# Optimization experiments

Measured on AMD Instinct MI355X. Metric: run time of the kernel, lower is better.

Reference implementation:

```python
import jax, jax.numpy as jnp
import numpy as np

N = 50000   # nodes of the target node type
E = 800000  # edges per incoming edge type (avg degree 16)
D = 128     # in == hidden == out channels (required by the module's pooling layer)


def sage_mean(x, edge_index, Wl, bl, Wr):
    """PyG SAGEConv with mean aggregation: lin_l(mean_j x_j) + lin_r(x_i).
    Note: per the original code, sources are gathered from the TARGET node
    feature table (x_input = x_dict[tgt_node_type])."""
    src, tgt = edge_index[0], edge_index[1]
    msg = x[src]                                                   # [E, D] gather
    agg = jax.ops.segment_sum(msg, tgt, num_segments=x.shape[0])   # [N, D] scatter-add
    cnt = jax.ops.segment_sum(jnp.ones((edge_index.shape[1],), x.dtype), tgt,
                              num_segments=x.shape[0])             # [N] degree
    agg = agg / jnp.maximum(cnt, 1.0)[:, None]                     # mean; 0 for isolated nodes
    return agg @ Wl + bl + x @ Wr                                  # [N, D]


def setup_inputs() -> dict:
    key = jax.random.key(0)
    ks = jax.random.split(key, 6)
    s = 1.0 / np.sqrt(D)
    x = jax.random.normal(ks[0], (N, D), jnp.float32)
    edge_index_a = jax.random.randint(ks[1], (2, E), 0, N)
    edge_index_b = jax.random.randint(ks[2], (2, E), 0, N)
    Wl = jax.random.normal(ks[3], (D, D), jnp.float32) * s
    Wr = jax.random.normal(ks[4], (D, D), jnp.float32) * s
    bl = jnp.zeros((D,), jnp.float32)
    Wp = jax.random.normal(ks[5], (D, D), jnp.float32) * s
    bp = jnp.zeros((D,), jnp.float32)
    return {"x": x, "Wl": Wl, "bl": bl, "Wr": Wr, "Wp": Wp, "bp": bp,
            "edge_index_a": edge_index_a, "edge_index_b": edge_index_b}


def reference(x, Wl, bl, Wr, Wp, bp, edge_index_a, edge_index_b):
    # One SAGEConv encoder + pooling Linear shared across incoming edge types,
    # softmax per edge type, then mean over edge types (torch.stack(...).mean(0)).
    outs = []
    for ei in (edge_index_a, edge_index_b):
        h = sage_mean(x, ei, Wl, bl, Wr)            # [N, D]
        outs.append(jax.nn.softmax(h @ Wp + bp, axis=-1))
    return (outs[0] + outs[1]) * 0.5                # [N, D]
```

## Files before the change

kernel.cpp:

```cpp
#include <hip/hip_runtime.h>
#include <math.h>

constexpr int D    = 128;
constexpr int BT   = 128;
constexpr int TILE = 4096;

using bf16x8 = __attribute__((ext_vector_type(8))) short;
using f32x4  = __attribute__((ext_vector_type(4))) float;
#define MFMA16 __builtin_amdgcn_mfma_f32_16x16x32_bf16

__device__ __forceinline__ unsigned short f2bf(float f) {
    unsigned u = __builtin_bit_cast(unsigned, f);
    u = (u + 0x7FFF + ((u >> 16) & 1)) >> 16;
    return (unsigned short)u;
}

__global__ __launch_bounds__(256)
void prep_kernel(const float* __restrict__ x, unsigned short* __restrict__ x_bfs,
                 const int* __restrict__ ea, int Ea,
                 const int* __restrict__ eb, int Eb,
                 unsigned int* __restrict__ ent_a, int* __restrict__ cnt_a,
                 unsigned int* __restrict__ ent_b, int* __restrict__ cnt_b,
                 const float* __restrict__ Wl, const float* __restrict__ Wr,
                 const float* __restrict__ Wp,
                 unsigned short* __restrict__ WlB, unsigned short* __restrict__ WrB,
                 unsigned short* __restrict__ WpB,
                 int N, int NBKT, int CAP, int GA, int GB, int GCONV)
{
    __shared__ int hist[512];
    __shared__ int base[512];

    const int bid = blockIdx.x;
    const int t   = threadIdx.x;

    if (bid < GA + GB) {
        const int type = (bid >= GA);
        const int* e   = type ? eb : ea;
        const int  E   = type ? Eb : Ea;
        unsigned int* ent = type ? ent_b : ent_a;
        int* cnt          = type ? cnt_b : cnt_a;
        const int i0 = (bid - type * GA) * TILE;

        for (int h = t; h < NBKT; h += 256) hist[h] = 0;
        __syncthreads();

        int tgts[16];
        #pragma unroll
        for (int j = 0; j < 16; ++j) {
            int i = i0 + j * 256 + t;
            tgts[j] = (i < E) ? e[(size_t)E + i] : -1;
            if (tgts[j] >= 0) atomicAdd(&hist[tgts[j] >> 7], 1);
        }
        __syncthreads();

        for (int h = t; h < NBKT; h += 256) {
            base[h] = (hist[h] > 0) ? atomicAdd(&cnt[h], hist[h]) : 0;
            hist[h] = 0;
        }
        __syncthreads();

        #pragma unroll
        for (int j = 0; j < 16; ++j) {
            int i = i0 + j * 256 + t;
            if (tgts[j] >= 0) {
                int b   = tgts[j] >> 7;
                int pos = base[b] + atomicAdd(&hist[b], 1);
                if (pos < CAP)
                    ent[(size_t)b * CAP + pos] = ((unsigned)e[i] << 7) | (tgts[j] & 127);
            }
        }
    } else if (bid < GA + GB + GCONV) {
        const int total4 = N * 32;
        for (int i = (bid - GA - GB) * 256 + t; i < total4; i += GCONV * 256) {
            int n  = i >> 5;
            int j4 = i & 31;
            float4 v = reinterpret_cast<const float4*>(x)[i];
            ushort4 o;
            o.x = f2bf(v.x); o.y = f2bf(v.y); o.z = f2bf(v.z); o.w = f2bf(v.w);
            int s = j4 >> 3, c = (j4 & 7) * 4;
            *reinterpret_cast<ushort4*>(x_bfs + ((size_t)s * N + n) * 32 + c) = o;
        }
    } else {
        int gw = ((bid - GA - GB - GCONV) * 256 + t) >> 6;
        int l  = t & 63;
        const float* W = (gw < 32) ? Wl : (gw < 64) ? Wr : Wp;
        unsigned short* O = (gw < 32) ? WlB : (gw < 64) ? WrB : WpB;
        int ktnt = gw & 31, kt = ktnt >> 3, nt = ktnt & 7;
        bf16x8 v;
        #pragma unroll
        for (int j = 0; j < 8; ++j)
            v[j] = (short)f2bf(W[(size_t)(kt * 32 + (l >> 4) * 8 + j) * D + nt * 16 + (l & 15)]);
        *reinterpret_cast<bf16x8*>(O + ((size_t)ktnt * 64 + l) * 8) = v;
    }
}

__global__ __launch_bounds__(512)
void sort_kernel(const unsigned int* __restrict__ ent_a, const int* __restrict__ cnt_a,
                 const unsigned int* __restrict__ ent_b, const int* __restrict__ cnt_b,
                 unsigned short* __restrict__ srcl_g, int* __restrict__ off_g,
                 int NBKT, int CAP)
{
    extern __shared__ __align__(16) char smem_raw[];
    int* tmp  = (int*)smem_raw;
    int* off  = tmp + CAP;
    int* cur  = off + BT + 1;
    int* wtot = cur + BT;
    unsigned short* srcl = (unsigned short*)(wtot + 2);

    const int bid  = blockIdx.x;
    const int type = (bid >= NBKT);
    const int k    = bid - type * NBKT;
    const unsigned int* ent = type ? ent_b : ent_a;
    const int cnt = min((type ? cnt_b : cnt_a)[k], CAP);

    const int t = threadIdx.x, l = t & 63, w = t >> 6;

    if (t < BT) off[t] = 0;
    __syncthreads();

    for (int i = t; i < cnt; i += 512) {
        unsigned e = ent[(size_t)k * CAP + i];
        tmp[i] = (int)e;
        atomicAdd(&off[e & (BT - 1)], 1);
    }
    __syncthreads();

    int v = 0, s = 0;
    if (t < BT) {
        v = off[t]; s = v;
        #pragma unroll
        for (int o = 1; o < 64; o <<= 1) {
            int u = __shfl_up(s, o, 64);
            if (l >= o) s += u;
        }
        if (l == 63) wtot[w] = s;
    }
    __syncthreads();
    if (t < BT) {
        int ex = ((w == 1) ? wtot[0] : 0) + s - v;
        off[t] = ex; cur[t] = ex;
    }
    if (t == 0) off[BT] = wtot[0] + wtot[1];
    __syncthreads();

    for (int i = t; i < cnt; i += 512) {
        unsigned e = (unsigned)tmp[i];
        int pos = atomicAdd(&cur[e & (BT - 1)], 1);
        srcl[pos] = (unsigned short)(e >> 7);
    }
    __syncthreads();

    for (int i = t; i < cnt; i += 512)
        srcl_g[(size_t)bid * CAP + i] = srcl[i];
    if (t <= BT)
        off_g[(size_t)bid * (BT + 1) + t] = off[t];
}

__global__ __launch_bounds__(256)
void gather_kernel(const unsigned short* __restrict__ x_bfs,
                   const unsigned short* __restrict__ srcl_g,
                   const int* __restrict__ off_g,
                   unsigned short* __restrict__ mean_a_s,
                   unsigned short* __restrict__ mean_b_s,
                   int N, int NBKT, int CAP)
{
    extern __shared__ __align__(16) char smem_raw[];
    int* off = (int*)smem_raw;
    unsigned short* srcl = (unsigned short*)(off + BT + 1);

    const int bid   = blockIdx.x;
    const int slice = bid & 3;
    const int tb    = bid >> 2;
    const int type  = (tb >= NBKT);
    const int k     = tb - type * NBKT;

    const int t = threadIdx.x, l = t & 63, w = t >> 6;
    const int q = l >> 4, c = l & 15;

    const int cnt = off_g[(size_t)tb * (BT + 1) + BT];
    for (int i = t; i <= BT; i += 256)
        off[i] = off_g[(size_t)tb * (BT + 1) + i];
    for (int i = t; i < cnt; i += 256)
        srcl[i] = srcl_g[(size_t)tb * CAP + i];
    __syncthreads();

    const unsigned short* xs = x_bfs + (size_t)slice * N * 32;
    unsigned short* mean = (type ? mean_b_s : mean_a_s) + (size_t)slice * N * 32;

    for (int tt = w; tt < BT; tt += 4) {
        const int n = k * BT + tt;
        if (n >= N) break;
        const int o0 = off[tt], o1 = off[tt + 1];
        float ax = 0.f, ay = 0.f;

        int j = o0 + q;
        for (; j + 4 < o1; j += 8) {
            int s0 = srcl[j], s1 = srcl[j + 4];
            unsigned v0 = *(const unsigned*)(xs + (size_t)s0 * 32 + c * 2);
            unsigned v1 = *(const unsigned*)(xs + (size_t)s1 * 32 + c * 2);
            ax += __builtin_bit_cast(float, v0 << 16)
                + __builtin_bit_cast(float, v1 << 16);
            ay += __builtin_bit_cast(float, v0 & 0xffff0000u)
                + __builtin_bit_cast(float, v1 & 0xffff0000u);
        }
        if (j < o1) {
            int s0 = srcl[j];
            unsigned v0 = *(const unsigned*)(xs + (size_t)s0 * 32 + c * 2);
            ax += __builtin_bit_cast(float, v0 << 16);
            ay += __builtin_bit_cast(float, v0 & 0xffff0000u);
        }

        ax += __shfl_xor(ax, 16, 64); ax += __shfl_xor(ax, 32, 64);
        ay += __shfl_xor(ay, 16, 64); ay += __shfl_xor(ay, 32, 64);

        float r = 1.0f / fmaxf((float)(o1 - o0), 1.0f);
        if (q == 0) {
            unsigned o = ((unsigned)f2bf(ay * r) << 16) | f2bf(ax * r);
            *(unsigned*)(mean + (size_t)n * 32 + c * 2) = o;
        }
    }
}

__global__ __launch_bounds__(256)
void gemm_kernel(const unsigned short* __restrict__ mean_a_s,
                 const unsigned short* __restrict__ mean_b_s,
                 const unsigned short* __restrict__ x_bfs,
                 const unsigned short* __restrict__ WlB,
                 const unsigned short* __restrict__ WrB,
                 const unsigned short* __restrict__ WpB,
                 const float* __restrict__ bl, const float* __restrict__ bp,
                 float* __restrict__ out, int N)
{
    __shared__ unsigned short hA[64 * D];
    __shared__ unsigned short hB[64 * D];

    const int t = threadIdx.x, w = t >> 6, l = t & 63;
    const int q = l & 15;
    const int kg = l >> 4;
    const int node0 = blockIdx.x * 64 + w * 16;
    const int arow = min(node0 + q, N - 1);

    bf16x8 fa[4], fb[4], fx[4];
    #pragma unroll
    for (int kt = 0; kt < 4; ++kt) {
        size_t o = ((size_t)kt * N + arow) * 32 + kg * 8;
        fa[kt] = *reinterpret_cast<const bf16x8*>(mean_a_s + o);
        fb[kt] = *reinterpret_cast<const bf16x8*>(mean_b_s + o);
        fx[kt] = *reinterpret_cast<const bf16x8*>(x_bfs + o);
    }

    #pragma unroll
    for (int nt = 0; nt < 8; ++nt) {
        f32x4 ca = {0.f, 0.f, 0.f, 0.f};
        f32x4 cb = {0.f, 0.f, 0.f, 0.f};
        #pragma unroll
        for (int kt = 0; kt < 4; ++kt) {
            const size_t fo = ((size_t)(kt * 8 + nt) * 64 + l) * 8;
            bf16x8 wl = *reinterpret_cast<const bf16x8*>(WlB + fo);
            bf16x8 wr = *reinterpret_cast<const bf16x8*>(WrB + fo);
            ca = MFMA16(fa[kt], wl, ca, 0, 0, 0);
            ca = MFMA16(fx[kt], wr, ca, 0, 0, 0);
            cb = MFMA16(fb[kt], wl, cb, 0, 0, 0);
            cb = MFMA16(fx[kt], wr, cb, 0, 0, 0);
        }
        float blv = bl[nt * 16 + q];
        #pragma unroll
        for (int r = 0; r < 4; ++r) {
            int lrow = w * 16 + kg * 4 + r;
            int byte = lrow * 256 + (nt * 16 + q) * 2;
            byte ^= ((lrow & 7) << 4);
            *reinterpret_cast<unsigned short*>(reinterpret_cast<char*>(hA) + byte) = f2bf(ca[r] + blv);
            *reinterpret_cast<unsigned short*>(reinterpret_cast<char*>(hB) + byte) = f2bf(cb[r] + blv);
        }
    }
    __syncthreads();

    bf16x8 ga[4], gb[4];
    #pragma unroll
    for (int kt = 0; kt < 4; ++kt) {
        int lrow = w * 16 + q;
        int byte = lrow * 256 + kt * 64 + kg * 16;
        byte ^= ((lrow & 7) << 4);
        ga[kt] = *reinterpret_cast<bf16x8*>(reinterpret_cast<char*>(hA) + byte);
        gb[kt] = *reinterpret_cast<bf16x8*>(reinterpret_cast<char*>(hB) + byte);
    }

    f32x4 la[8], lb[8];
    #pragma unroll
    for (int nt = 0; nt < 8; ++nt) {
        la[nt] = f32x4{0.f, 0.f, 0.f, 0.f};
        lb[nt] = f32x4{0.f, 0.f, 0.f, 0.f};
        #pragma unroll
        for (int kt = 0; kt < 4; ++kt) {
            const size_t fo = ((size_t)(kt * 8 + nt) * 64 + l) * 8;
            bf16x8 wp = *reinterpret_cast<const bf16x8*>(WpB + fo);
            la[nt] = MFMA16(ga[kt], wp, la[nt], 0, 0, 0);
            lb[nt] = MFMA16(gb[kt], wp, lb[nt], 0, 0, 0);
        }
        float bpv = bp[nt * 16 + q];
        #pragma unroll
        for (int r = 0; r < 4; ++r) { la[nt][r] += bpv; lb[nt][r] += bpv; }
    }

    #pragma unroll
    for (int r = 0; r < 4; ++r) {
        float ma = -INFINITY, mb = -INFINITY;
        #pragma unroll
        for (int nt = 0; nt < 8; ++nt) {
            ma = fmaxf(ma, la[nt][r]);
            mb = fmaxf(mb, lb[nt][r]);
        }
        #pragma unroll
        for (int o = 1; o < 16; o <<= 1) {
            ma = fmaxf(ma, __shfl_xor(ma, o, 64));
            mb = fmaxf(mb, __shfl_xor(mb, o, 64));
        }
        float ea[8], eb[8], sa = 0.f, sb = 0.f;
        #pragma unroll
        for (int nt = 0; nt < 8; ++nt) {
            ea[nt] = __expf(la[nt][r] - ma); sa += ea[nt];
            eb[nt] = __expf(lb[nt][r] - mb); sb += eb[nt];
        }
        #pragma unroll
        for (int o = 1; o < 16; o <<= 1) {
            sa += __shfl_xor(sa, o, 64);
            sb += __shfl_xor(sb, o, 64);
        }
        float ra = 0.5f / sa, rb = 0.5f / sb;
        int grow = node0 + kg * 4 + r;
        if (grow < N) {
            float* o = out + (size_t)grow * D + q;
            #pragma unroll
            for (int nt = 0; nt < 8; ++nt)
                o[nt * 16] = ea[nt] * ra + eb[nt] * rb;
        }
    }
}

extern "C" void kernel_launch(void* const* d_in, const int* in_sizes, int n_in,
                              void* d_out, int out_size, void* d_ws, size_t ws_size,
                              hipStream_t stream)
{
    const float* x  = (const float*)d_in[0];
    const float* Wl = (const float*)d_in[1];
    const float* bl = (const float*)d_in[2];
    const float* Wr = (const float*)d_in[3];
    const float* Wp = (const float*)d_in[4];
    const float* bp = (const float*)d_in[5];
    const int*   ea = (const int*)d_in[6];
    const int*   eb = (const int*)d_in[7];

    const int N  = in_sizes[0] / D;
    const int Ea = in_sizes[6] / 2;
    const int Eb = in_sizes[7] / 2;

    const int NBKT = (N + BT - 1) / BT;
    const int Emax = Ea > Eb ? Ea : Eb;
    int CAP = (int)(((long long)Emax * BT / N) * 5 / 4 + 128);
    CAP = (CAP + 7) & ~7;

    unsigned int* ent_a = (unsigned int*)d_ws;
    unsigned int* ent_b = ent_a + (size_t)NBKT * CAP;
    int* cnt_a = (int*)(ent_b + (size_t)NBKT * CAP);
    int* cnt_b = cnt_a + NBKT;
    int* off_g = cnt_b + NBKT;
    uintptr_t p = (uintptr_t)(off_g + (size_t)2 * NBKT * (BT + 1));
    p = (p + 15) & ~(uintptr_t)15;
    unsigned short* srcl_g  = (unsigned short*)p;
    unsigned short* x_bfs   = srcl_g + (size_t)2 * NBKT * CAP;
    unsigned short* mean_a_s = x_bfs + (size_t)N * D;
    unsigned short* mean_b_s = mean_a_s + (size_t)N * D;
    unsigned short* WlB     = mean_b_s + (size_t)N * D;
    unsigned short* WrB     = WlB + D * D;
    unsigned short* WpB     = WrB + D * D;

    hipMemsetAsync(cnt_a, 0, sizeof(int) * 2 * (size_t)NBKT, stream);

    const int GA = (Ea + TILE - 1) / TILE;
    const int GB = (Eb + TILE - 1) / TILE;
    const int GCONV = 512;
    prep_kernel<<<GA + GB + GCONV + 24, 256, 0, stream>>>(
        x, x_bfs, ea, Ea, eb, Eb, ent_a, cnt_a, ent_b, cnt_b,
        Wl, Wr, Wp, WlB, WrB, WpB, N, NBKT, CAP, GA, GB, GCONV);

    const int smem_sort = CAP * 6 + (BT + 1 + BT + 2) * 4 + 16;
    sort_kernel<<<2 * NBKT, 512, smem_sort, stream>>>(
        ent_a, cnt_a, ent_b, cnt_b, srcl_g, off_g, NBKT, CAP);

    const int smem_gather = (BT + 1) * 4 + CAP * 2 + 16;
    gather_kernel<<<8 * NBKT, 256, smem_gather, stream>>>(
        x_bfs, srcl_g, off_g, mean_a_s, mean_b_s, N, NBKT, CAP);

    gemm_kernel<<<(N + 63) / 64, 256, 0, stream>>>(
        mean_a_s, mean_b_s, x_bfs, WlB, WrB, WpB, bl, bp, (float*)d_out, N);
}
```

Before: 150.7 us.

## Fold Wp into SAGE weights and aggregate projected features instead of raw x

Precomputes Wl·Wp and Wr·Wp (plus folded bias) in a small kernel, so each node's features are projected once by a dense GEMM before aggregation. Because mean aggregation is linear, the gather now averages projected rows, and a light epilogue only adds the root term and applies the softmax. The large second GEMM stage and the per-type duplicated GEMMs are removed. It adds an extra kernel launch and intermediate bf16 buffers, and the gather is restructured so each wave handles four nodes in lockstep up to the maximum degree. Rounding the fused weights and projected features to bf16 may change numerics slightly.

Measured after the change: 176.2 us. +16.9%, slower.

```diff
diff --git a/kernel.cpp b/kernel.cpp
--- a/kernel.cpp
+++ b/kernel.cpp
@@ -16,15 +16,65 @@
 }
 
 __global__ __launch_bounds__(256)
-void prep_kernel(const float* __restrict__ x, unsigned short* __restrict__ x_bfs,
+void wprod_kernel(const float* __restrict__ Wl, const float* __restrict__ Wr,
+                  const float* __restrict__ Wp,
+                  const float* __restrict__ bl, const float* __restrict__ bp,
+                  unsigned short* __restrict__ WlpB, unsigned short* __restrict__ WrpB,
+                  float* __restrict__ cvec)
+{
+    __shared__ float wm[128 * 128];
+    __shared__ float wp[128 * 128];
+
+    const float* Wm = blockIdx.x ? Wr : Wl;
+    unsigned short* OB = blockIdx.x ? WrpB : WlpB;
+    const int t = threadIdx.x;
+
+    for (int i = t; i < 4096; i += 256) {
+        reinterpret_cast<float4*>(wm)[i] = reinterpret_cast<const float4*>(Wm)[i];
+        reinterpret_cast<float4*>(wp)[i] = reinterpret_cast<const float4*>(Wp)[i];
+    }
+    __syncthreads();
+
+    const int w = t >> 6, l = t & 63;
+    const int r0 = w * 32 + (l >> 4) * 8;
+    const int c0 = l & 15;
+
+    float acc[8][8];
+    #pragma unroll
+    for (int j = 0; j < 8; ++j)
+        #pragma unroll
+        for (int nt = 0; nt < 8; ++nt) acc[j][nt] = 0.f;
+
+    for (int k = 0; k < 128; ++k) {
+        float wpv[8];
+        #pragma unroll
+        for (int nt = 0; nt < 8; ++nt) wpv[nt] = wp[k * 128 + nt * 16 + c0];
+        #pragma unroll
+        for (int j = 0; j < 8; ++j) {
+            float wmv = wm[(r0 + j) * 128 + k];
+            #pragma unroll
+            for (int nt = 0; nt < 8; ++nt) acc[j][nt] += wmv * wpv[nt];
+        }
+    }
+    #pragma unroll
+    for (int nt = 0; nt < 8; ++nt)
+        #pragma unroll
+        for (int j = 0; j < 8; ++j)
+            OB[((size_t)(w * 8 + nt) * 64 + l) * 8 + j] = f2bf(acc[j][nt]);
+
+    if (blockIdx.x == 0 && t < 128) {
+        float s = bp[t];
+        for (int k = 0; k < 128; ++k) s += bl[k] * wp[k * 128 + t];
+        cvec[t] = s;
+    }
+}
+
+__global__ __launch_bounds__(256)
+void prep_kernel(const float* __restrict__ x, unsigned short* __restrict__ x_bf,
                  const int* __restrict__ ea, int Ea,
                  const int* __restrict__ eb, int Eb,
                  unsigned int* __restrict__ ent_a, int* __restrict__ cnt_a,
                  unsigned int* __restrict__ ent_b, int* __restrict__ cnt_b,
-                 const float* __restrict__ Wl, const float* __restrict__ Wr,
-                 const float* __restrict__ Wp,
-                 unsigned short* __restrict__ WlB, unsigned short* __restrict__ WrB,
-                 unsigned short* __restrict__ WpB,
                  int N, int NBKT, int CAP, int GA, int GB, int GCONV)
 {
     __shared__ int hist[512];
@@ -69,28 +119,14 @@
                     ent[(size_t)b * CAP + pos] = ((unsigned)e[i] << 7) | (tgts[j] & 127);
             }
         }
-    } else if (bid < GA + GB + GCONV) {
+    } else {
         const int total4 = N * 32;
         for (int i = (bid - GA - GB) * 256 + t; i < total4; i += GCONV * 256) {
-            int n  = i >> 5;
-            int j4 = i & 31;
             float4 v = reinterpret_cast<const float4*>(x)[i];
             ushort4 o;
             o.x = f2bf(v.x); o.y = f2bf(v.y); o.z = f2bf(v.z); o.w = f2bf(v.w);
-            int s = j4 >> 3, c = (j4 & 7) * 4;
-            *reinterpret_cast<ushort4*>(x_bfs + ((size_t)s * N + n) * 32 + c) = o;
-        }
-    } else {
-        int gw = ((bid - GA - GB - GCONV) * 256 + t) >> 6;
-        int l  = t & 63;
-        const float* W = (gw < 32) ? Wl : (gw < 64) ? Wr : Wp;
-        unsigned short* O = (gw < 32) ? WlB : (gw < 64) ? WrB : WpB;
-        int ktnt = gw & 31, kt = ktnt >> 3, nt = ktnt & 7;
-        bf16x8 v;
-        #pragma unroll
-        for (int j = 0; j < 8; ++j)
-            v[j] = (short)f2bf(W[(size_t)(kt * 32 + (l >> 4) * 8 + j) * D + nt * 16 + (l & 15)]);
-        *reinterpret_cast<bf16x8*>(O + ((size_t)ktnt * 64 + l) * 8) = v;
+            reinterpret_cast<ushort4*>(x_bf)[i] = o;
+        }
     }
 }
 
@@ -157,11 +193,55 @@
 }
 
 __global__ __launch_bounds__(256)
-void gather_kernel(const unsigned short* __restrict__ x_bfs,
+void gemmz_kernel(const unsigned short* __restrict__ x_bf,
+                  const unsigned short* __restrict__ WlpB,
+                  const unsigned short* __restrict__ WrpB,
+                  const float* __restrict__ cvec,
+                  unsigned short* __restrict__ zl, unsigned short* __restrict__ zr,
+                  int N)
+{
+    const int t = threadIdx.x, w = t >> 6, l = t & 63;
+    const int q = l & 15, kg = l >> 4;
+    const int node0 = blockIdx.x * 64 + w * 16;
+    const int arow = min(node0 + q, N - 1);
+
+    bf16x8 fx[4];
+    #pragma unroll
+    for (int kt = 0; kt < 4; ++kt)
+        fx[kt] = *reinterpret_cast<const bf16x8*>(x_bf + (size_t)arow * D + kt * 32 + kg * 8);
+
+    #pragma unroll
+    for (int nt = 0; nt < 8; ++nt) {
+        f32x4 cl = {0.f, 0.f, 0.f, 0.f};
+        f32x4 cr = {0.f, 0.f, 0.f, 0.f};
+        #pragma unroll
+        for (int kt = 0; kt < 4; ++kt) {
+            const size_t fo = ((size_t)(kt * 8 + nt) * 64 + l) * 8;
+            bf16x8 wl = *reinterpret_cast<const bf16x8*>(WlpB + fo);
+            bf16x8 wr = *reinterpret_cast<const bf16x8*>(WrpB + fo);
+            cl = MFMA16(fx[kt], wl, cl, 0, 0, 0);
+            cr = MFMA16(fx[kt], wr, cr, 0, 0, 0);
+        }
+        float cv = cvec[nt * 16 + q];
+        const int sidx = nt >> 1;
+        const int cin  = (nt & 1) * 16 + q;
+        #pragma unroll
+        for (int r = 0; r < 4; ++r) {
+            int grow = node0 + kg * 4 + r;
+            if (grow < N) {
+                zl[((size_t)sidx * N + grow) * 32 + cin] = f2bf(cl[r]);
+                zr[(size_t)grow * D + nt * 16 + q]       = f2bf(cr[r] + cv);
+            }
+        }
+    }
+}
+
+__global__ __launch_bounds__(256)
+void gather_kernel(const unsigned* __restrict__ zl,
                    const unsigned short* __restrict__ srcl_g,
                    const int* __restrict__ off_g,
-                   unsigned short* __restrict__ mean_a_s,
-                   unsigned short* __restrict__ mean_b_s,
+                   unsigned short* __restrict__ agg_a,
+                   unsigned short* __restrict__ agg_b,
                    int N, int NBKT, int CAP)
 {
     extern __shared__ __align__(16) char smem_raw[];
@@ -175,7 +255,8 @@
     const int k     = tb - type * NBKT;
 
     const int t = threadIdx.x, l = t & 63, w = t >> 6;
-    const int q = l >> 4, c = l & 15;
+    const int q = l >> 4;
+    const unsigned c = l & 15;
 
     const int cnt = off_g[(size_t)tb * (BT + 1) + BT];
     for (int i = t; i <= BT; i += 256)
@@ -184,157 +265,99 @@
         srcl[i] = srcl_g[(size_t)tb * CAP + i];
     __syncthreads();
 
-    const unsigned short* xs = x_bfs + (size_t)slice * N * 32;
-    unsigned short* mean = (type ? mean_b_s : mean_a_s) + (size_t)slice * N * 32;
-
-    for (int tt = w; tt < BT; tt += 4) {
+    const unsigned* zs = zl + (size_t)slice * N * 16;
+    unsigned short* agg = (type ? agg_b : agg_a) + (size_t)slice * N * 32;
+
+    #pragma unroll
+    for (int pass = 0; pass < BT / 16; ++pass) {
+        const int tt = pass * 16 + w * 4 + q;
+        const int o0 = off[tt], o1 = off[tt + 1];
+        const int deg = o1 - o0;
+        int md = max(deg, __shfl_xor(deg, 16, 64));
+        md = max(md, __shfl_xor(md, 32, 64));
+
+        float a0 = 0.f, a1 = 0.f;
+        #pragma unroll 4
+        for (int j = 0; j < md; ++j) {
+            const bool act = (j < deg);
+            const int idx = o0 + (act ? j : 0);
+            const unsigned s = srcl[idx];
+            const unsigned v = zs[s * 16 + c];
+            if (act) {
+                a0 += __builtin_bit_cast(float, v << 16);
+                a1 += __builtin_bit_cast(float, v & 0xffff0000u);
+            }
+        }
+        const float r = 1.0f / fmaxf((float)deg, 1.0f);
         const int n = k * BT + tt;
-        if (n >= N) break;
-        const int o0 = off[tt], o1 = off[tt + 1];
-        float ax = 0.f, ay = 0.f;
-
-        int j = o0 + q;
-        for (; j + 4 < o1; j += 8) {
-            int s0 = srcl[j], s1 = srcl[j + 4];
-            unsigned v0 = *(const unsigned*)(xs + (size_t)s0 * 32 + c * 2);
-            unsigned v1 = *(const unsigned*)(xs + (size_t)s1 * 32 + c * 2);
-            ax += __builtin_bit_cast(float, v0 << 16)
-                + __builtin_bit_cast(float, v1 << 16);
-            ay += __builtin_bit_cast(float, v0 & 0xffff0000u)
-                + __builtin_bit_cast(float, v1 & 0xffff0000u);
-        }
-        if (j < o1) {
-            int s0 = srcl[j];
-            unsigned v0 = *(const unsigned*)(xs + (size_t)s0 * 32 + c * 2);
-            ax += __builtin_bit_cast(float, v0 << 16);
-            ay += __builtin_bit_cast(float, v0 & 0xffff0000u);
-        }
-
-        ax += __shfl_xor(ax, 16, 64); ax += __shfl_xor(ax, 32, 64);
-        ay += __shfl_xor(ay, 16, 64); ay += __shfl_xor(ay, 32, 64);
-
-        float r = 1.0f / fmaxf((float)(o1 - o0), 1.0f);
-        if (q == 0) {
-            unsigned o = ((unsigned)f2bf(ay * r) << 16) | f2bf(ax * r);
-            *(unsigned*)(mean + (size_t)n * 32 + c * 2) = o;
+        if (n < N) {
+            unsigned o = ((unsigned)f2bf(a1 * r) << 16) | f2bf(a0 * r);
+            *(unsigned*)(agg + (size_t)n * 32 + c * 2) = o;
         }
     }
 }
 
 __global__ __launch_bounds__(256)
-void gemm_kernel(const unsigned short* __restrict__ mean_a_s,
-                 const unsigned short* __restrict__ mean_b_s,
-                 const unsigned short* __restrict__ x_bfs,
-                 const unsigned short* __restrict__ WlB,
-                 const unsigned short* __restrict__ WrB,
-                 const unsigned short* __restrict__ WpB,
-                 const float* __restrict__ bl, const float* __restrict__ bp,
-                 float* __restrict__ out, int N)
-{
-    __shared__ unsigned short hA[64 * D];
-    __shared__ unsigned short hB[64 * D];
-
-    const int t = threadIdx.x, w = t >> 6, l = t & 63;
-    const int q = l & 15;
-    const int kg = l >> 4;
-    const int node0 = blockIdx.x * 64 + w * 16;
-    const int arow = min(node0 + q, N - 1);
-
-    bf16x8 fa[4], fb[4], fx[4];
-    #pragma unroll
-    for (int kt = 0; kt < 4; ++kt) {
-        size_t o = ((size_t)kt * N + arow) * 32 + kg * 8;
-        fa[kt] = *reinterpret_cast<const bf16x8*>(mean_a_s + o);
-        fb[kt] = *reinterpret_cast<const bf16x8*>(mean_b_s + o);
-        fx[kt] = *reinterpret_cast<const bf16x8*>(x_bfs + o);
-    }
-
-    #pragma unroll
-    for (int nt = 0; nt < 8; ++nt) {
-        f32x4 ca = {0.f, 0.f, 0.f, 0.f};
-        f32x4 cb = {0.f, 0.f, 0.f, 0.f};
-        #pragma unroll
-        for (int kt = 0; kt < 4; ++kt) {
-            const size_t fo = ((size_t)(kt * 8 + nt) * 64 + l) * 8;
-            bf16x8 wl = *reinterpret_cast<const bf16x8*>(WlB + fo);
-            bf16x8 wr = *reinterpret_cast<const bf16x8*>(WrB + fo);
-            ca = MFMA16(fa[kt], wl, ca, 0, 0, 0);
-            ca = MFMA16(fx[kt], wr, ca, 0, 0, 0);
-            cb = MFMA16(fb[kt], wl, cb, 0, 0, 0);
-            cb = MFMA16(fx[kt], wr, cb, 0, 0, 0);
-        }
-        float blv = bl[nt * 16 + q];
-        #pragma unroll
-        for (int r = 0; r < 4; ++r) {
-            int lrow = w * 16 + kg * 4 + r;
-            int byte = lrow * 256 + (nt * 16 + q) * 2;
-            byte ^= ((lrow & 7) << 4);
-            *reinterpret_cast<unsigned short*>(reinterpret_cast<char*>(hA) + byte) = f2bf(ca[r] + blv);
-            *reinterpret_cast<unsigned short*>(reinterpret_cast<char*>(hB) + byte) = f2bf(cb[r] + blv);
-        }
-    }
-    __syncthreads();
-
-    bf16x8 ga[4], gb[4];
-    #pragma unroll
-    for (int kt = 0; kt < 4; ++kt) {
-        int lrow = w * 16 + q;
-        int byte = lrow * 256 + kt * 64 + kg * 16;
-        byte ^= ((lrow & 7) << 4);
-        ga[kt] = *reinterpret_cast<bf16x8*>(reinterpret_cast<char*>(hA) + byte);
-        gb[kt] = *reinterpret_cast<bf16x8*>(reinterpret_cast<char*>(hB) + byte);
-    }
-
-    f32x4 la[8], lb[8];
-    #pragma unroll
-    for (int nt = 0; nt < 8; ++nt) {
-        la[nt] = f32x4{0.f, 0.f, 0.f, 0.f};
-        lb[nt] = f32x4{0.f, 0.f, 0.f, 0.f};
-        #pragma unroll
-        for (int kt = 0; kt < 4; ++kt) {
-            const size_t fo = ((size_t)(kt * 8 + nt) * 64 + l) * 8;
-            bf16x8 wp = *reinterpret_cast<const bf16x8*>(WpB + fo);
-            la[nt] = MFMA16(ga[kt], wp, la[nt], 0, 0, 0);
-            lb[nt] = MFMA16(gb[kt], wp, lb[nt], 0, 0, 0);
-        }
-        float bpv = bp[nt * 16 + q];
-        #pragma unroll
-        for (int r = 0; r < 4; ++r) { la[nt][r] += bpv; lb[nt][r] += bpv; }
-    }
-
-    #pragma unroll
-    for (int r = 0; r < 4; ++r) {
-        float ma = -INFINITY, mb = -INFINITY;
-        #pragma unroll
-        for (int nt = 0; nt < 8; ++nt) {
-            ma = fmaxf(ma, la[nt][r]);
-            mb = fmaxf(mb, lb[nt][r]);
-        }
-        #pragma unroll
-        for (int o = 1; o < 16; o <<= 1) {
-            ma = fmaxf(ma, __shfl_xor(ma, o, 64));
-            mb = fmaxf(mb, __shfl_xor(mb, o, 64));
-        }
-        float ea[8], eb[8], sa = 0.f, sb = 0.f;
-        #pragma unroll
-        for (int nt = 0; nt < 8; ++nt) {
-            ea[nt] = __expf(la[nt][r] - ma); sa += ea[nt];
-            eb[nt] = __expf(lb[nt][r] - mb); sb += eb[nt];
-        }
-        #pragma unroll
-        for (int o = 1; o < 16; o <<= 1) {
-            sa += __shfl_xor(sa, o, 64);
-            sb += __shfl_xor(sb, o, 64);
-        }
-        float ra = 0.5f / sa, rb = 0.5f / sb;
-        int grow = node0 + kg * 4 + r;
-        if (grow < N) {
-            float* o = out + (size_t)grow * D + q;
-            #pragma unroll
-            for (int nt = 0; nt < 8; ++nt)
-                o[nt * 16] = ea[nt] * ra + eb[nt] * rb;
-        }
-    }
+void epi_kernel(const unsigned short* __restrict__ agg_a,
+                const unsigned short* __restrict__ agg_b,
+                const unsigned short* __restrict__ zr,
+                float* __restrict__ out, int N)
+{
+    const int t = threadIdx.x;
+    const int n = blockIdx.x * 16 + (t >> 4);
+    const int c = t & 15;
+    if (n >= N) return;
+
+    const int s = c >> 2;
+    const size_t aoff = ((size_t)s * N + n) * 32 + (c & 3) * 8;
+    uint4 va = *reinterpret_cast<const uint4*>(agg_a + aoff);
+    uint4 vb = *reinterpret_cast<const uint4*>(agg_b + aoff);
+    uint4 vz = *reinterpret_cast<const uint4*>(zr + (size_t)n * D + c * 8);
+
+    unsigned ua[4] = {va.x, va.y, va.z, va.w};
+    unsigned ub[4] = {vb.x, vb.y, vb.z, vb.w};
+    unsigned uz[4] = {vz.x, vz.y, vz.z, vz.w};
+
+    float la[8], lb[8];
+    #pragma unroll
+    for (int d = 0; d < 4; ++d) {
+        float z0 = __builtin_bit_cast(float, uz[d] << 16);
+        float z1 = __builtin_bit_cast(float, uz[d] & 0xffff0000u);
+        la[2*d]   = __builtin_bit_cast(float, ua[d] << 16) + z0;
+        la[2*d+1] = __builtin_bit_cast(float, ua[d] & 0xffff0000u) + z1;
+        lb[2*d]   = __builtin_bit_cast(float, ub[d] << 16) + z0;
+        lb[2*d+1] = __builtin_bit_cast(float, ub[d] & 0xffff0000u) + z1;
+    }
+
+    float ma = -INFINITY, mb = -INFINITY;
+    #pragma unroll
+    for (int j = 0; j < 8; ++j) { ma = fmaxf(ma, la[j]); mb = fmaxf(mb, lb[j]); }
+    #pragma unroll
+    for (int o = 1; o < 16; o <<= 1) {
+        ma = fmaxf(ma, __shfl_xor(ma, o, 64));
+        mb = fmaxf(mb, __shfl_xor(mb, o, 64));
+    }
+    float sa = 0.f, sb = 0.f;
+    #pragma unroll
+    for (int j = 0; j < 8; ++j) {
+        la[j] = __expf(la[j] - ma); sa += la[j];
+        lb[j] = __expf(lb[j] - mb); sb += lb[j];
+    }
+    #pragma unroll
+    for (int o = 1; o < 16; o <<= 1) {
+        sa += __shfl_xor(sa, o, 64);
+        sb += __shfl_xor(sb, o, 64);
+    }
+    const float ra = 0.5f / sa, rb = 0.5f / sb;
+
+    float4 o0, o1;
+    o0.x = la[0]*ra + lb[0]*rb; o0.y = la[1]*ra + lb[1]*rb;
+    o0.z = la[2]*ra + lb[2]*rb; o0.w = la[3]*ra + lb[3]*rb;
+    o1.x = la[4]*ra + lb[4]*rb; o1.y = la[5]*ra + lb[5]*rb;
+    o1.z = la[6]*ra + lb[6]*rb; o1.w = la[7]*ra + lb[7]*rb;
+    float* op = out + (size_t)n * D + c * 8;
+    *reinterpret_cast<float4*>(op)     = o0;
+    *reinterpret_cast<float4*>(op + 4) = o1;
 }
 
 extern "C" void kernel_launch(void* const* d_in, const int* in_sizes, int n_in,
@@ -364,33 +387,40 @@
     int* cnt_a = (int*)(ent_b + (size_t)NBKT * CAP);
     int* cnt_b = cnt_a + NBKT;
     int* off_g = cnt_b + NBKT;
-    uintptr_t p = (uintptr_t)(off_g + (size_t)2 * NBKT * (BT + 1));
+    float* cvec = (float*)(off_g + (size_t)2 * NBKT * (BT + 1));
+    uintptr_t p = (uintptr_t)(cvec + 128);
     p = (p + 15) & ~(uintptr_t)15;
-    unsigned short* srcl_g  = (unsigned short*)p;
-    unsigned short* x_bfs   = srcl_g + (size_t)2 * NBKT * CAP;
-    unsigned short* mean_a_s = x_bfs + (size_t)N * D;
-    unsigned short* mean_b_s = mean_a_s + (size_t)N * D;
-    unsigned short* WlB     = mean_b_s + (size_t)N * D;
-    unsigned short* WrB     = WlB + D * D;
-    unsigned short* WpB     = WrB + D * D;
+    unsigned short* srcl_g = (unsigned short*)p;
+    unsigned short* x_bf   = srcl_g + (size_t)2 * NBKT * CAP;
+    unsigned short* zl     = x_bf + (size_t)N * D;
+    unsigned short* zr     = zl + (size_t)N * D;
+    unsigned short* agg_a  = zr + (size_t)N * D;
+    unsigned short* agg_b  = agg_a + (size_t)N * D;
+    unsigned short* WlpB   = agg_b + (size_t)N * D;
+    unsigned short* WrpB   = WlpB + D * D;
 
     hipMemsetAsync(cnt_a, 0, sizeof(int) * 2 * (size_t)NBKT, stream);
+
+    wprod_kernel<<<2, 256, 0, stream>>>(Wl, Wr, Wp, bl, bp, WlpB, WrpB, cvec);
 
     const int GA = (Ea + TILE - 1) / TILE;
     const int GB = (Eb + TILE - 1) / TILE;
     const int GCONV = 512;
-    prep_kernel<<<GA + GB + GCONV + 24, 256, 0, stream>>>(
-        x, x_bfs, ea, Ea, eb, Eb, ent_a, cnt_a, ent_b, cnt_b,
-        Wl, Wr, Wp, WlB, WrB, WpB, N, NBKT, CAP, GA, GB, GCONV);
+    prep_kernel<<<GA + GB + GCONV, 256, 0, stream>>>(
+        x, x_bf, ea, Ea, eb, Eb, ent_a, cnt_a, ent_b, cnt_b,
+        N, NBKT, CAP, GA, GB, GCONV);
 
     const int smem_sort = CAP * 6 + (BT + 1 + BT + 2) * 4 + 16;
     sort_kernel<<<2 * NBKT, 512, smem_sort, stream>>>(
         ent_a, cnt_a, ent_b, cnt_b, srcl_g, off_g, NBKT, CAP);
 
+    gemmz_kernel<<<(N + 63) / 64, 256, 0, stream>>>(
+        x_bf, WlpB, WrpB, cvec, zl, zr, N);
+
     const int smem_gather = (BT + 1) * 4 + CAP * 2 + 16;
     gather_kernel<<<8 * NBKT, 256, smem_gather, stream>>>(
-        x_bfs, srcl_g, off_g, mean_a_s, mean_b_s, N, NBKT, CAP);
-
-    gemm_kernel<<<(N + 63) / 64, 256, 0, stream>>>(
-        mean_a_s, mean_b_s, x_bfs, WlB, WrB, WpB, bl, bp, (float*)d_out, N);
-}
+        (const unsigned*)zl, srcl_g, off_g, agg_a, agg_b, N, NBKT, CAP);
+
+    epi_kernel<<<(N + 15) / 16, 256, 0, stream>>>(agg_a, agg_b, zr,
+                                                  (float*)d_out, N);
+}
```
